# Kernel optimization log

Hardware: AMD Instinct MI355X
Metric: run time of the kernel (lower is better)

The kernel has to match this reference:

```python
import jax, jax.numpy as jnp
import numpy as np

NLEVELS = 16
FEATURES = 2
TABLE_SIZE = 2 ** 18
MINRES, MAXRES = 16, 512
_b = (MAXRES / MINRES) ** (1.0 / (NLEVELS - 1))
RES = [int(np.floor(MINRES * _b ** l + 1e-6)) for l in range(NLEVELS)]
# Instant-NGP spatial hash primes (first prime is 1)
PRIMES = np.array([1, 2654435761, 805459861], dtype=np.uint32)


def _interp(coords, res, gather):
    """Trilinear interpolation. coords: [N,3] in [-1,1]; gather: [N,3]int -> [N,F]."""
    pos = jnp.clip((coords + 1.0) * 0.5 * (res - 1), 0.0, res - 1)  # [N,3] grid coords
    i0 = jnp.floor(pos)
    w = pos - i0                              # [N,3] fractional weights
    i0 = i0.astype(jnp.int32)
    out = jnp.zeros((coords.shape[0], FEATURES), coords.dtype)
    for corner in range(8):                   # 8 trilinear corners
        off = jnp.array([(corner >> 2) & 1, (corner >> 1) & 1, corner & 1], jnp.int32)
        idx = jnp.minimum(i0 + off, res - 1)  # clamp at boundary ('nearest' padding)
        wgt = jnp.prod(jnp.where(off == 1, w, 1.0 - w), axis=-1)  # [N]
        out = out + gather(idx) * wgt[:, None]
    return out  # [N, F]


def setup_inputs() -> dict:
    key = jax.random.key(0)
    k1, k2, k3 = jax.random.split(key, 3)
    N = 2 ** 21
    coords = jax.random.uniform(k1, (N, 3), jnp.float32, -1.0, 1.0)
    dense_grid = jax.random.uniform(k2, (FEATURES, RES[0], RES[0], RES[0]), jnp.float32, -1e-4, 1e-4)
    hash_tables = jax.random.uniform(k3, (NLEVELS - 1, FEATURES, TABLE_SIZE), jnp.float32, -1e-4, 1e-4)
    return {"coords": coords, "dense_grid": dense_grid, "hash_tables": hash_tables}


def reference(coords, dense_grid, hash_tables):
    feats = []
    R0 = RES[0]
    gflat = dense_grid.reshape(FEATURES, -1)  # [F, R0^3]

    def dense_gather(idx):
        flat = (idx[:, 0] * R0 + idx[:, 1]) * R0 + idx[:, 2]
        return gflat[:, flat].T               # [N, F]

    feats.append(_interp(coords, R0, dense_gather))

    primes = jnp.asarray(PRIMES)
    for l in range(1, NLEVELS):
        table = hash_tables[l - 1]            # [F, T]

        def hash_gather(idx, table=table):
            u = idx.astype(jnp.uint32) * primes
            h = (u[:, 0] ^ u[:, 1] ^ u[:, 2]) % TABLE_SIZE
            return table[:, h].T              # [N, F]

        feats.append(_interp(coords, RES[l], hash_gather))

    return jnp.concatenate(feats, axis=-1)    # [N, NLEVELS*FEATURES]
```

## Files before the change

### kernel.cpp

```cpp
#include <hip/hip_runtime.h>

#define TS 262144
#define TMASK (TS - 1)
#define P2 2654435761u
#define P3 805459861u

__global__ __launch_bounds__(256) void xpose_kernel(
    const float* __restrict__ dense, const float* __restrict__ tables,
    float2* __restrict__ ws) {
  int i = blockIdx.x * 256 + threadIdx.x;
  const int total = 15 * TS;
  if (i < total) {
    int l = i >> 18;
    int h = i & TMASK;
    const float* t = tables + (size_t)l * (2 * TS);
    ws[4096 + i] = make_float2(t[h], t[TS + h]);
  } else {
    int j = i - total;
    if (j < 4096) ws[j] = make_float2(dense[j], dense[4096 + j]);
  }
}

template <bool XP>
__global__ __launch_bounds__(256) void encode_kernel(
    const float* __restrict__ coords,
    const float* __restrict__ dense,
    const float* __restrict__ tables,
    const float2* __restrict__ xtab,
    float4* __restrict__ out, int npts) {
  constexpr int RESA[16] = {16, 20, 25, 32, 40, 50, 64, 80,
                            101, 128, 161, 203, 256, 322, 406, 512};
  __shared__ float s_c[768];
  const int tid = threadIdx.x;
  const int pbase = blockIdx.x * 256;

#pragma unroll
  for (int j = 0; j < 3; ++j) {
    int gi = pbase * 3 + j * 256 + tid;
    s_c[j * 256 + tid] = (gi < npts * 3) ? __builtin_nontemporal_load(&coords[gi]) : 0.0f;
  }
  __syncthreads();

  const int n = pbase + tid;
  const bool valid = n < npts;
  const float cxn = (s_c[tid * 3 + 0] + 1.0f) * 0.5f;
  const float cyn = (s_c[tid * 3 + 1] + 1.0f) * 0.5f;
  const float czn = (s_c[tid * 3 + 2] + 1.0f) * 0.5f;

  float acc[32];

#pragma unroll
  for (int lvl = 0; lvl < 16; ++lvl) {
    const int res = RESA[lvl];
    const int r1 = res - 1;
    const float rm1 = (float)r1;

    float px = fminf(fmaxf(cxn * rm1, 0.0f), rm1);
    float py = fminf(fmaxf(cyn * rm1, 0.0f), rm1);
    float pz = fminf(fmaxf(czn * rm1, 0.0f), rm1);
    float fx = floorf(px), fy = floorf(py), fz = floorf(pz);
    float wx = px - fx, wy = py - fy, wz = pz - fz;
    int ix0 = (int)fx, iy0 = (int)fy, iz0 = (int)fz;
    int ix1 = min(ix0 + 1, r1), iy1 = min(iy0 + 1, r1), iz1 = min(iz0 + 1, r1);

    unsigned hx0, hx1, hy0, hy1, hz0, hz1;
    if (lvl == 0) {
      hx0 = (unsigned)ix0 << 8; hx1 = (unsigned)ix1 << 8;
      hy0 = (unsigned)iy0 << 4; hy1 = (unsigned)iy1 << 4;
      hz0 = (unsigned)iz0;      hz1 = (unsigned)iz1;
    } else {
      hx0 = (unsigned)ix0;      hx1 = (unsigned)ix1;
      hy0 = (unsigned)iy0 * P2; hy1 = (unsigned)iy1 * P2;
      hz0 = (unsigned)iz0 * P3; hz1 = (unsigned)iz1 * P3;
    }

    unsigned idx[8];
    float wgt[8];
#pragma unroll
    for (int c = 0; c < 8; ++c) {
      unsigned hx = (c & 4) ? hx1 : hx0;
      unsigned hy = (c & 2) ? hy1 : hy0;
      unsigned hz = (c & 1) ? hz1 : hz0;
      idx[c] = (hx ^ hy ^ hz) & TMASK;
      float a = (c & 4) ? wx : 1.0f - wx;
      float b = (c & 2) ? wy : 1.0f - wy;
      float d = (c & 1) ? wz : 1.0f - wz;
      wgt[c] = a * b * d;
    }

    float a0 = 0.0f, a1 = 0.0f;
    if (XP) {
      const float2* tab = (lvl == 0) ? xtab : (xtab + 4096 + (size_t)(lvl - 1) * TS);
      float2 v[8];
#pragma unroll
      for (int c = 0; c < 8; ++c) v[c] = tab[idx[c]];
#pragma unroll
      for (int c = 0; c < 8; ++c) {
        a0 = fmaf(v[c].x, wgt[c], a0);
        a1 = fmaf(v[c].y, wgt[c], a1);
      }
    } else {
      const float* t0 = (lvl == 0) ? dense : (tables + (size_t)(lvl - 1) * (2 * TS));
      const unsigned fs = (lvl == 0) ? 4096u : (unsigned)TS;
      float v0[8], v1[8];
#pragma unroll
      for (int c = 0; c < 8; ++c) { v0[c] = t0[idx[c]]; v1[c] = t0[fs + idx[c]]; }
#pragma unroll
      for (int c = 0; c < 8; ++c) {
        a0 = fmaf(v0[c], wgt[c], a0);
        a1 = fmaf(v1[c], wgt[c], a1);
      }
    }
    acc[2 * lvl + 0] = a0;
    acc[2 * lvl + 1] = a1;

    __syncthreads();
  }

  if (valid) {
    float4* o = out + (size_t)n * 8;
#pragma unroll
    for (int j = 0; j < 8; ++j)
      o[j] = make_float4(acc[4 * j + 0], acc[4 * j + 1], acc[4 * j + 2], acc[4 * j + 3]);
  }
}

extern "C" void kernel_launch(void* const* d_in, const int* in_sizes, int n_in,
                              void* d_out, int out_size, void* d_ws, size_t ws_size,
                              hipStream_t stream) {
  const float* coords = (const float*)d_in[0];
  const float* dense  = (const float*)d_in[1];
  const float* tables = (const float*)d_in[2];
  float4* out = (float4*)d_out;
  const int npts = in_sizes[0] / 3;
  const int eblocks = (npts + 255) / 256;
  const size_t need = (size_t)(4096 + 15 * TS) * sizeof(float2);

  if (ws_size >= need) {
    float2* ws = (float2*)d_ws;
    const int tblocks = (15 * TS + 4096 + 255) / 256;
    hipLaunchKernelGGL(xpose_kernel, dim3(tblocks), dim3(256), 0, stream,
                       dense, tables, ws);
    hipLaunchKernelGGL((encode_kernel<true>), dim3(eblocks), dim3(256), 0, stream,
                       coords, dense, tables, ws, out, npts);
  } else {
    hipLaunchKernelGGL((encode_kernel<false>), dim3(eblocks), dim3(256), 0, stream,
                       coords, dense, tables, (const float2*)nullptr, out, npts);
  }
}
```

Before: 1.498 ms.

## Precompute dense z-pair float4 tables for coarse levels to halve gathers

Measured after the change: 1.919 ms. 28.1% more time.

```diff
diff --git a/kernel.cpp b/kernel.cpp
--- a/kernel.cpp
+++ b/kernel.cpp
@@ -5,19 +5,55 @@
 #define P2 2654435761u
 #define P3 805459861u
 
-__global__ __launch_bounds__(256) void xpose_kernel(
+typedef float nfloat4 __attribute__((ext_vector_type(4)));
+
+#define N4 511633
+
+__global__ __launch_bounds__(256) void build_kernel(
     const float* __restrict__ dense, const float* __restrict__ tables,
-    float2* __restrict__ ws) {
+    float4* __restrict__ ws4) {
   int i = blockIdx.x * 256 + threadIdx.x;
-  const int total = 15 * TS;
-  if (i < total) {
-    int l = i >> 18;
-    int h = i & TMASK;
-    const float* t = tables + (size_t)l * (2 * TS);
-    ws[4096 + i] = make_float2(t[h], t[TS + h]);
+  if (i < N4) {
+    constexpr int OFF4[8] = {0, 4096, 12096, 27721, 60489, 124489, 249489, N4};
+    constexpr int RESL[7] = {16, 20, 25, 32, 40, 50, 64};
+    int lvl = 0;
+#pragma unroll
+    for (int l = 1; l < 7; ++l)
+      if (i >= OFF4[l]) lvl = l;
+    int j = i - OFF4[lvl];
+    int res = RESL[lvl];
+    int z = j % res;
+    int t = j / res;
+    int y = t % res;
+    int x = t / res;
+    int zp = min(z + 1, res - 1);
+    float f0a, f1a, f0b, f1b;
+    if (lvl == 0) {
+      int i0 = (x * 16 + y) * 16 + z;
+      int i1 = (x * 16 + y) * 16 + zp;
+      f0a = dense[i0];
+      f1a = dense[4096 + i0];
+      f0b = dense[i1];
+      f1b = dense[4096 + i1];
+    } else {
+      const float* tb = tables + (size_t)(lvl - 1) * (2 * TS);
+      unsigned h0 = ((unsigned)x ^ ((unsigned)y * P2) ^ ((unsigned)z * P3)) & TMASK;
+      unsigned h1 = ((unsigned)x ^ ((unsigned)y * P2) ^ ((unsigned)zp * P3)) & TMASK;
+      f0a = tb[h0];
+      f1a = tb[TS + h0];
+      f0b = tb[h1];
+      f1b = tb[TS + h1];
+    }
+    ws4[i] = make_float4(f0a, f1a, f0b, f1b);
   } else {
-    int j = i - total;
-    if (j < 4096) ws[j] = make_float2(dense[j], dense[4096 + j]);
+    int i2 = i - N4;
+    if (i2 < 9 * TS) {
+      int l = i2 >> 18;
+      int h = i2 & TMASK;
+      const float* tb = tables + (size_t)(l + 6) * (2 * TS);
+      float2* ws2 = (float2*)(ws4 + N4);
+      ws2[i2] = make_float2(tb[h], tb[TS + h]);
+    }
   }
 }
 
@@ -26,10 +62,11 @@
     const float* __restrict__ coords,
     const float* __restrict__ dense,
     const float* __restrict__ tables,
-    const float2* __restrict__ xtab,
+    const float4* __restrict__ xt4,
     float4* __restrict__ out, int npts) {
   constexpr int RESA[16] = {16, 20, 25, 32, 40, 50, 64, 80,
                             101, 128, 161, 203, 256, 322, 406, 512};
+  constexpr int OFF4[7] = {0, 4096, 12096, 27721, 60489, 124489, 249489};
   __shared__ float s_c[768];
   const int tid = threadIdx.x;
   const int pbase = blockIdx.x * 256;
@@ -61,54 +98,79 @@
     float fx = floorf(px), fy = floorf(py), fz = floorf(pz);
     float wx = px - fx, wy = py - fy, wz = pz - fz;
     int ix0 = (int)fx, iy0 = (int)fy, iz0 = (int)fz;
-    int ix1 = min(ix0 + 1, r1), iy1 = min(iy0 + 1, r1), iz1 = min(iz0 + 1, r1);
-
-    unsigned hx0, hx1, hy0, hy1, hz0, hz1;
-    if (lvl == 0) {
-      hx0 = (unsigned)ix0 << 8; hx1 = (unsigned)ix1 << 8;
-      hy0 = (unsigned)iy0 << 4; hy1 = (unsigned)iy1 << 4;
-      hz0 = (unsigned)iz0;      hz1 = (unsigned)iz1;
+    int ix1 = min(ix0 + 1, r1), iy1 = min(iy0 + 1, r1);
+
+    float a0 = 0.0f, a1 = 0.0f;
+    if (XP && lvl < 7) {
+      const float4* __restrict__ tab = xt4 + OFF4[lvl];
+      int b00 = (ix0 * res + iy0) * res + iz0;
+      int b01 = (ix0 * res + iy1) * res + iz0;
+      int b10 = (ix1 * res + iy0) * res + iz0;
+      int b11 = (ix1 * res + iy1) * res + iz0;
+      float4 v00 = tab[b00];
+      float4 v01 = tab[b01];
+      float4 v10 = tab[b10];
+      float4 v11 = tab[b11];
+      float w00 = (1.0f - wx) * (1.0f - wy), w01 = (1.0f - wx) * wy;
+      float w10 = wx * (1.0f - wy), w11 = wx * wy;
+      float z0 = 1.0f - wz, z1 = wz;
+      a0 = v00.x * (w00 * z0);            a1 = v00.y * (w00 * z0);
+      a0 = fmaf(v00.z, w00 * z1, a0);     a1 = fmaf(v00.w, w00 * z1, a1);
+      a0 = fmaf(v01.x, w01 * z0, a0);     a1 = fmaf(v01.y, w01 * z0, a1);
+      a0 = fmaf(v01.z, w01 * z1, a0);     a1 = fmaf(v01.w, w01 * z1, a1);
+      a0 = fmaf(v10.x, w10 * z0, a0);     a1 = fmaf(v10.y, w10 * z0, a1);
+      a0 = fmaf(v10.z, w10 * z1, a0);     a1 = fmaf(v10.w, w10 * z1, a1);
+      a0 = fmaf(v11.x, w11 * z0, a0);     a1 = fmaf(v11.y, w11 * z0, a1);
+      a0 = fmaf(v11.z, w11 * z1, a0);     a1 = fmaf(v11.w, w11 * z1, a1);
     } else {
-      hx0 = (unsigned)ix0;      hx1 = (unsigned)ix1;
-      hy0 = (unsigned)iy0 * P2; hy1 = (unsigned)iy1 * P2;
-      hz0 = (unsigned)iz0 * P3; hz1 = (unsigned)iz1 * P3;
-    }
-
-    unsigned idx[8];
-    float wgt[8];
-#pragma unroll
-    for (int c = 0; c < 8; ++c) {
-      unsigned hx = (c & 4) ? hx1 : hx0;
-      unsigned hy = (c & 2) ? hy1 : hy0;
-      unsigned hz = (c & 1) ? hz1 : hz0;
-      idx[c] = (hx ^ hy ^ hz) & TMASK;
-      float a = (c & 4) ? wx : 1.0f - wx;
-      float b = (c & 2) ? wy : 1.0f - wy;
-      float d = (c & 1) ? wz : 1.0f - wz;
-      wgt[c] = a * b * d;
-    }
-
-    float a0 = 0.0f, a1 = 0.0f;
-    if (XP) {
-      const float2* tab = (lvl == 0) ? xtab : (xtab + 4096 + (size_t)(lvl - 1) * TS);
-      float2 v[8];
-#pragma unroll
-      for (int c = 0; c < 8; ++c) v[c] = tab[idx[c]];
+      int iz1 = min(iz0 + 1, r1);
+      unsigned hx0, hx1, hy0, hy1, hz0, hz1;
+      if (lvl == 0) {
+        hx0 = (unsigned)ix0 << 8; hx1 = (unsigned)ix1 << 8;
+        hy0 = (unsigned)iy0 << 4; hy1 = (unsigned)iy1 << 4;
+        hz0 = (unsigned)iz0;      hz1 = (unsigned)iz1;
+      } else {
+        hx0 = (unsigned)ix0;      hx1 = (unsigned)ix1;
+        hy0 = (unsigned)iy0 * P2; hy1 = (unsigned)iy1 * P2;
+        hz0 = (unsigned)iz0 * P3; hz1 = (unsigned)iz1 * P3;
+      }
+
+      unsigned idx[8];
+      float wgt[8];
 #pragma unroll
       for (int c = 0; c < 8; ++c) {
-        a0 = fmaf(v[c].x, wgt[c], a0);
-        a1 = fmaf(v[c].y, wgt[c], a1);
+        unsigned hx = (c & 4) ? hx1 : hx0;
+        unsigned hy = (c & 2) ? hy1 : hy0;
+        unsigned hz = (c & 1) ? hz1 : hz0;
+        idx[c] = (hx ^ hy ^ hz) & TMASK;
+        float a = (c & 4) ? wx : 1.0f - wx;
+        float b = (c & 2) ? wy : 1.0f - wy;
+        float d = (c & 1) ? wz : 1.0f - wz;
+        wgt[c] = a * b * d;
       }
-    } else {
-      const float* t0 = (lvl == 0) ? dense : (tables + (size_t)(lvl - 1) * (2 * TS));
-      const unsigned fs = (lvl == 0) ? 4096u : (unsigned)TS;
-      float v0[8], v1[8];
-#pragma unroll
-      for (int c = 0; c < 8; ++c) { v0[c] = t0[idx[c]]; v1[c] = t0[fs + idx[c]]; }
-#pragma unroll
-      for (int c = 0; c < 8; ++c) {
-        a0 = fmaf(v0[c], wgt[c], a0);
-        a1 = fmaf(v1[c], wgt[c], a1);
+
+      if (XP) {
+        const float2* __restrict__ tab =
+            ((const float2*)(xt4 + N4)) + (size_t)(lvl - 7) * TS;
+        float2 v[8];
+#pragma unroll
+        for (int c = 0; c < 8; ++c) v[c] = tab[idx[c]];
+#pragma unroll
+        for (int c = 0; c < 8; ++c) {
+          a0 = fmaf(v[c].x, wgt[c], a0);
+          a1 = fmaf(v[c].y, wgt[c], a1);
+        }
+      } else {
+        const float* t0 = (lvl == 0) ? dense : (tables + (size_t)(lvl - 1) * (2 * TS));
+        const unsigned fs = (lvl == 0) ? 4096u : (unsigned)TS;
+        float v0[8], v1[8];
+#pragma unroll
+        for (int c = 0; c < 8; ++c) { v0[c] = t0[idx[c]]; v1[c] = t0[fs + idx[c]]; }
+#pragma unroll
+        for (int c = 0; c < 8; ++c) {
+          a0 = fmaf(v0[c], wgt[c], a0);
+          a1 = fmaf(v1[c], wgt[c], a1);
+        }
       }
     }
     acc[2 * lvl + 0] = a0;
@@ -118,10 +180,12 @@
   }
 
   if (valid) {
-    float4* o = out + (size_t)n * 8;
-#pragma unroll
-    for (int j = 0; j < 8; ++j)
-      o[j] = make_float4(acc[4 * j + 0], acc[4 * j + 1], acc[4 * j + 2], acc[4 * j + 3]);
+    nfloat4* o = (nfloat4*)(out + (size_t)n * 8);
+#pragma unroll
+    for (int j = 0; j < 8; ++j) {
+      nfloat4 v = {acc[4 * j + 0], acc[4 * j + 1], acc[4 * j + 2], acc[4 * j + 3]};
+      __builtin_nontemporal_store(v, o + j);
+    }
   }
 }
 
@@ -134,17 +198,18 @@
   float4* out = (float4*)d_out;
   const int npts = in_sizes[0] / 3;
   const int eblocks = (npts + 255) / 256;
-  const size_t need = (size_t)(4096 + 15 * TS) * sizeof(float2);
+  const size_t need = (size_t)N4 * sizeof(float4) + (size_t)9 * TS * sizeof(float2);
 
   if (ws_size >= need) {
-    float2* ws = (float2*)d_ws;
-    const int tblocks = (15 * TS + 4096 + 255) / 256;
-    hipLaunchKernelGGL(xpose_kernel, dim3(tblocks), dim3(256), 0, stream,
-                       dense, tables, ws);
+    float4* ws4 = (float4*)d_ws;
+    const int total = N4 + 9 * TS;
+    const int tblocks = (total + 255) / 256;
+    hipLaunchKernelGGL(build_kernel, dim3(tblocks), dim3(256), 0, stream,
+                       dense, tables, ws4);
     hipLaunchKernelGGL((encode_kernel<true>), dim3(eblocks), dim3(256), 0, stream,
-                       coords, dense, tables, ws, out, npts);
+                       coords, dense, tables, ws4, out, npts);
   } else {
     hipLaunchKernelGGL((encode_kernel<false>), dim3(eblocks), dim3(256), 0, stream,
-                       coords, dense, tables, (const float2*)nullptr, out, npts);
+                       coords, dense, tables, (const float4*)nullptr, out, npts);
   }
 }
```
